# Kernel optimization log

Measured on AMD Instinct MI355X. Metric: run time of the kernel, lower is better.

Reference implementation:

```python
import jax, jax.numpy as jnp
import numpy as np

DIM = 64
H = 4
POS_DIM = 4
NUM_IDS = 16
B = 2048
N = 64


def setup_inputs() -> dict:
    key = jax.random.key(0)
    ks = jax.random.split(key, 16)
    d8 = DIM // 8
    stdv = 1.0 / np.sqrt(DIM * DIM)
    inp = {
        "x": jax.random.normal(ks[0], (B, N, DIM), jnp.float32),
        "pos": jax.random.normal(ks[1], (B, N, POS_DIM), jnp.float32),
        "strength": jax.random.normal(ks[2], (512,), jnp.float32),
        "embed_id1": 3,
        # weights stored [in, out] (torch Linear weight transposed)
        "Wq": jax.random.normal(ks[3], (DIM, DIM), jnp.float32) * 0.05,
        "Wk": jax.random.normal(ks[4], (DIM, DIM), jnp.float32) * 0.05,
        "pos_W1": jax.random.normal(ks[5], (POS_DIM, POS_DIM), jnp.float32) * 0.3,
        "pos_b1": jnp.zeros((POS_DIM,), jnp.float32),
        "pos_W2": jax.random.normal(ks[6], (POS_DIM, d8), jnp.float32) * 0.3,
        "pos_b2": jnp.zeros((d8,), jnp.float32),
        "head_W": jax.random.normal(ks[7], (d8, H), jnp.float32) * 0.3,
        "head_b": jnp.zeros((H,), jnp.float32),
        "gate": jnp.ones((H,), jnp.float32),
        "embeds": jax.random.uniform(ks[8], (NUM_IDS, DIM * DIM), jnp.float32, -stdv, stdv),
        "out_W": jax.random.normal(ks[9], (DIM, DIM), jnp.float32) * 0.05,
        "out_b": jnp.zeros((DIM,), jnp.float32),
        "str_W": jax.random.normal(ks[10], (512, 64), jnp.float32) * 0.04,
        "str_b": jnp.zeros((64,), jnp.float32),
    }
    return inp


def reference(x, pos, strength, embed_id1, Wq, Wk, pos_W1, pos_b1, pos_W2, pos_b2,
              head_W, head_b, gate, embeds, out_W, out_b, str_W, str_b):
    Bb, Nn, dim = x.shape
    h = gate.shape[0]
    dh = dim // h

    # strength projection, added to dynamic-weight V
    s64 = strength @ str_W + str_b                       # [dim]
    E = embeds[embed_id1].reshape(dim, dim)              # per-sample V weight
    v = x @ E.T + s64                                    # F.linear(x, E) + strength
    v = v.reshape(Bb, Nn, h, dh).transpose(0, 2, 1, 3)   # [B,H,N,dh]

    # QK attention
    q = (x @ Wq).reshape(Bb, Nn, h, dh).transpose(0, 2, 1, 3)
    k = (x @ Wk).reshape(Bb, Nn, h, dh).transpose(0, 2, 1, 3)
    attn = jax.nn.softmax(jnp.einsum('bhqd,bhkd->bhqk', q, k) / np.sqrt(dh), axis=-1)

    # pairwise relative-position attention
    p = jax.nn.relu(pos @ pos_W1 + pos_b1) @ pos_W2 + pos_b2          # [B,N,dim//8]
    diff = p[:, :, None, :] - p[:, None, :, :]                        # [B,N,N,dim//8]
    pos_logits = jnp.einsum('bqkf,fh->bhqk', diff, head_W) + head_b[None, :, None, None]
    pos_attn = jax.nn.softmax(pos_logits, axis=-1)

    # sigmoid-gated mixing + renormalization
    g = jax.nn.sigmoid(gate)[None, :, None, None]
    attn = (1.0 - g) * attn + g * pos_attn
    attn = attn / jnp.sum(attn, axis=-1, keepdims=True)

    out = jnp.einsum('bhqk,bhkd->bhqd', attn, v)
    out = out.transpose(0, 2, 1, 3).reshape(Bb, Nn, dim)
    return out @ out_W + out_b
```

## Files before the change

kernel.cpp:

```cpp
#include <hip/hip_runtime.h>

typedef unsigned short u16;
typedef unsigned int u32;
typedef short bf8 __attribute__((ext_vector_type(8)));
typedef float f4v __attribute__((ext_vector_type(4)));
typedef float f16v __attribute__((ext_vector_type(16)));

#define STR 72

__device__ __forceinline__ u32 f2bf(float f){
    union{float f;u32 i;}c; c.f=f; u32 i=c.i;
    return (i + 0x7FFFu + ((i>>16)&1u)) >> 16;
}

__device__ __forceinline__ void stage_row16(const float* __restrict__ g, short* __restrict__ dst,
                                            int n, int c0){
    const float4* p = (const float4*)(g + n*64 + c0);
    float4 a=p[0], b=p[1], c=p[2], d=p[3];
    uint4 o0, o1;
    o0.x = f2bf(a.x)|(f2bf(a.y)<<16); o0.y = f2bf(a.z)|(f2bf(a.w)<<16);
    o0.z = f2bf(b.x)|(f2bf(b.y)<<16); o0.w = f2bf(b.z)|(f2bf(b.w)<<16);
    o1.x = f2bf(c.x)|(f2bf(c.y)<<16); o1.y = f2bf(c.z)|(f2bf(c.w)<<16);
    o1.z = f2bf(d.x)|(f2bf(d.y)<<16); o1.w = f2bf(d.z)|(f2bf(d.w)<<16);
    *(uint4*)&dst[n*STR + c0]     = o0;
    *(uint4*)&dst[n*STR + c0 + 8] = o1;
}

__global__ __launch_bounds__(256) void pre_kernel(
    const int* __restrict__ embed_id,
    const float* __restrict__ Wq, const float* __restrict__ Wk, const float* __restrict__ oW,
    const float* __restrict__ embeds, const float* __restrict__ sW, const float* __restrict__ sb,
    const float* __restrict__ strength,
    float* __restrict__ ws_s64, u16* __restrict__ ws_wq, u16* __restrict__ ws_wk,
    u16* __restrict__ ws_ow, u16* __restrict__ ws_e)
{
    const int j = blockIdx.x;
    const int t = threadIdx.x;

    if (j < 3) {
        const float* W = (j==0) ? Wq : (j==1) ? Wk : oW;
        u16* dst = (j==0) ? ws_wq : (j==1) ? ws_wk : ws_ow;
        const float scl = (j==0) ? 0.25f : 1.0f;
        const int kp = t >> 3, ng = t & 7;
        const float4* r0 = (const float4*)(W + (2*kp  )*64 + 8*ng);
        const float4* r1 = (const float4*)(W + (2*kp+1)*64 + 8*ng);
        float4 a0=r0[0], a1=r0[1], b0=r1[0], b1=r1[1];
        float lo[8]={a0.x,a0.y,a0.z,a0.w,a1.x,a1.y,a1.z,a1.w};
        float hi[8]={b0.x,b0.y,b0.z,b0.w,b1.x,b1.y,b1.z,b1.w};
        #pragma unroll
        for (int i=0;i<8;++i)
            *(u32*)&dst[(8*ng+i)*64 + 2*kp] = f2bf(scl*lo[i]) | (f2bf(scl*hi[i])<<16);
    } else {
        __shared__ float sp[4][64];
        {
            const int n = t >> 2, c0 = (t & 3) << 4;
            const float4* p = (const float4*)(embeds + (size_t)(*embed_id)*4096 + n*64 + c0);
            float4 a=p[0], b=p[1], c=p[2], d=p[3];
            uint4 o0, o1;
            o0.x = f2bf(a.x)|(f2bf(a.y)<<16); o0.y = f2bf(a.z)|(f2bf(a.w)<<16);
            o0.z = f2bf(b.x)|(f2bf(b.y)<<16); o0.w = f2bf(b.z)|(f2bf(b.w)<<16);
            o1.x = f2bf(c.x)|(f2bf(c.y)<<16); o1.y = f2bf(c.z)|(f2bf(c.w)<<16);
            o1.z = f2bf(d.x)|(f2bf(d.y)<<16); o1.w = f2bf(d.z)|(f2bf(d.w)<<16);
            *(uint4*)&ws_e[n*64 + c0]     = o0;
            *(uint4*)&ws_e[n*64 + c0 + 8] = o1;
        }
        {
            const int d = t & 63, part = t >> 6;
            const float* wp = sW + part*128*64 + d;
            const float* s  = strength + part*128;
            float acc = 0.f;
            #pragma unroll 8
            for (int i = 0; i < 128; ++i) acc = fmaf(s[i], wp[i*64], acc);
            sp[part][d] = acc;
        }
        __syncthreads();
        if (t < 64) ws_s64[t] = sp[0][t] + sp[1][t] + sp[2][t] + sp[3][t] + sb[t];
    }
}

__global__ __launch_bounds__(256, 3) void attn_main_kernel(
    const float* __restrict__ x, const float* __restrict__ pos,
    const float* __restrict__ gate, const float* __restrict__ ob,
    const float* __restrict__ pW1, const float* __restrict__ pb1,
    const float* __restrict__ pW2, const float* __restrict__ pb2,
    const float* __restrict__ hW,
    const float* __restrict__ ws_s64,
    const u16* __restrict__ ws_wq, const u16* __restrict__ ws_wk,
    const u16* __restrict__ ws_ow, const u16* __restrict__ ws_e,
    float* __restrict__ out)
{
    __shared__ short B0[64*STR];
    __shared__ short PX[64*STR];
    __shared__ short B2[64*STR];
    __shared__ short B3[64*STR];
    __shared__ short VT[64*STR];
    __shared__ float pat_l[4][64];

    const int t    = threadIdx.x;
    const int b    = blockIdx.x;
    const int lane = t & 63;
    const int w    = t >> 6;
    const int l15  = lane & 15;
    const int l31  = lane & 31;
    const int l5   = lane >> 5;
    const int quad = lane >> 4;
    const int n    = t >> 2;
    const int c0   = (t & 3) << 4;

    const int wq_off = (16*w + l15)*64 + quad*8;
    bf8 bq0 = *(const bf8*)&ws_wq[wq_off];
    bf8 bq1 = *(const bf8*)&ws_wq[wq_off + 32];
    bf8 bk0 = *(const bf8*)&ws_wk[wq_off];
    bf8 bk1 = *(const bf8*)&ws_wk[wq_off + 32];
    bf8 be0 = *(const bf8*)&ws_e [wq_off];
    bf8 be1 = *(const bf8*)&ws_e [wq_off + 32];
    bf8 bo0 = *(const bf8*)&ws_ow[wq_off];
    bf8 bo1 = *(const bf8*)&ws_ow[wq_off + 32];
    const float sv  = ws_s64[16*w + l15];
    const float obv = ob[16*w + l15];

    stage_row16(x + (size_t)b*4096, B0, n, c0);

    float g = 1.f/(1.f + __expf(-gate[w]));
    {
        const float4 pv = *(const float4*)(pos + ((size_t)b*64 + lane)*4);
        float h1[4], p8[8];
        #pragma unroll
        for (int jj = 0; jj < 4; ++jj){
            float a = pb1[jj];
            a = fmaf(pv.x, pW1[0*4+jj], a);
            a = fmaf(pv.y, pW1[1*4+jj], a);
            a = fmaf(pv.z, pW1[2*4+jj], a);
            a = fmaf(pv.w, pW1[3*4+jj], a);
            h1[jj] = fmaxf(a, 0.f);
        }
        #pragma unroll
        for (int f = 0; f < 8; ++f){
            float a = pb2[f];
            #pragma unroll
            for (int jj = 0; jj < 4; ++jj) a = fmaf(h1[jj], pW2[jj*8+f], a);
            p8[f] = a;
        }
        float tv = 0.f;
        #pragma unroll
        for (int f = 0; f < 8; ++f) tv = fmaf(p8[f], hW[f*4+w], tv);
        float v0 = -tv;
        float m = v0;
        #pragma unroll
        for (int off = 32; off; off >>= 1) m = fmaxf(m, __shfl_xor(m, off));
        float e = __expf(v0 - m);
        float ssum = e;
        #pragma unroll
        for (int off = 32; off; off >>= 1) ssum += __shfl_xor(ssum, off);
        pat_l[w][lane] = g * (e / ssum);
    }
    __syncthreads();

    #pragma unroll
    for (int mt=0; mt<4; ++mt){
        bf8 a0 = *(const bf8*)&B0[(16*mt + l15)*STR + quad*8];
        bf8 a1 = *(const bf8*)&B0[(16*mt + l15)*STR + 32 + quad*8];
        f4v cq, ck, cv;
        #pragma unroll
        for (int r=0;r<4;++r){ cq[r]=0.f; ck[r]=0.f; cv[r]=sv; }
        cq = __builtin_amdgcn_mfma_f32_16x16x32_bf16(a0, bq0, cq, 0,0,0);
        cq = __builtin_amdgcn_mfma_f32_16x16x32_bf16(a1, bq1, cq, 0,0,0);
        ck = __builtin_amdgcn_mfma_f32_16x16x32_bf16(a0, bk0, ck, 0,0,0);
        ck = __builtin_amdgcn_mfma_f32_16x16x32_bf16(a1, bk1, ck, 0,0,0);
        cv = __builtin_amdgcn_mfma_f32_16x16x32_bf16(a0, be0, cv, 0,0,0);
        cv = __builtin_amdgcn_mfma_f32_16x16x32_bf16(a1, be1, cv, 0,0,0);
        #pragma unroll
        for (int r=0;r<4;++r){
            B2[(16*mt + quad*4 + r)*STR + 16*w + l15] = (short)f2bf(cq[r]);
            B3[(16*mt + quad*4 + r)*STR + 16*w + l15] = (short)f2bf(ck[r]);
        }
        uint2 pk;
        pk.x = f2bf(cv[0]) | (f2bf(cv[1])<<16);
        pk.y = f2bf(cv[2]) | (f2bf(cv[3])<<16);
        *(uint2*)&VT[(16*w + l15)*STR + 16*mt + quad*4] = pk;
    }
    asm volatile("" ::: "memory");

    f16v S[2][2];
    {
        bf8 ka0 = *(const bf8*)&B3[(     l31)*STR + 16*w + 8*l5];
        bf8 ka1 = *(const bf8*)&B3[(32 + l31)*STR + 16*w + 8*l5];
        bf8 qb0 = *(const bf8*)&B2[(     l31)*STR + 16*w + 8*l5];
        bf8 qb1 = *(const bf8*)&B2[(32 + l31)*STR + 16*w + 8*l5];
        #pragma unroll
        for (int mt=0;mt<2;++mt)
            #pragma unroll
            for (int nt=0;nt<2;++nt)
                #pragma unroll
                for (int i=0;i<16;++i) S[mt][nt][i] = 0.f;
        S[0][0] = __builtin_amdgcn_mfma_f32_32x32x16_bf16(ka0, qb0, S[0][0], 0,0,0);
        S[0][1] = __builtin_amdgcn_mfma_f32_32x32x16_bf16(ka0, qb1, S[0][1], 0,0,0);
        S[1][0] = __builtin_amdgcn_mfma_f32_32x32x16_bf16(ka1, qb0, S[1][0], 0,0,0);
        S[1][1] = __builtin_amdgcn_mfma_f32_32x32x16_bf16(ka1, qb1, S[1][1], 0,0,0);
    }
    float inv_[2];
    #pragma unroll
    for (int nt=0;nt<2;++nt){
        float m = S[0][nt][0];
        #pragma unroll
        for (int i=1;i<16;++i) m = fmaxf(m, S[0][nt][i]);
        #pragma unroll
        for (int i=0;i<16;++i) m = fmaxf(m, S[1][nt][i]);
        m = fmaxf(m, __shfl_xor(m, 32));
        float l = 0.f;
        #pragma unroll
        for (int mt=0;mt<2;++mt)
            #pragma unroll
            for (int i=0;i<16;++i){ float e = __expf(S[mt][nt][i]-m); S[mt][nt][i] = e; l += e; }
        l += __shfl_xor(l, 32);
        float c1 = (1.f - g) / l;
        float tot = 0.f;
        #pragma unroll
        for (int mt=0;mt<2;++mt)
            #pragma unroll
            for (int rg=0;rg<4;++rg){
                const float4 tv = *(const float4*)&pat_l[w][32*mt + 8*rg + 4*l5];
                float a0 = fmaf(c1, S[mt][nt][rg*4+0], tv.x);
                float a1 = fmaf(c1, S[mt][nt][rg*4+1], tv.y);
                float a2 = fmaf(c1, S[mt][nt][rg*4+2], tv.z);
                float a3 = fmaf(c1, S[mt][nt][rg*4+3], tv.w);
                S[mt][nt][rg*4+0]=a0; S[mt][nt][rg*4+1]=a1;
                S[mt][nt][rg*4+2]=a2; S[mt][nt][rg*4+3]=a3;
                tot += a0+a1+a2+a3;
            }
        tot += __shfl_xor(tot, 32);
        inv_[nt] = 1.f / tot;
    }
    __syncthreads();

    short* Pb = (w==0) ? B0 : (w==1) ? PX : (w==2) ? B2 : B3;
    #pragma unroll
    for (int nt=0;nt<2;++nt)
        #pragma unroll
        for (int mt=0;mt<2;++mt)
            #pragma unroll
            for (int rg=0;rg<4;++rg){
                float v0 = S[mt][nt][rg*4+0]*inv_[nt], v1 = S[mt][nt][rg*4+1]*inv_[nt];
                float v2 = S[mt][nt][rg*4+2]*inv_[nt], v3 = S[mt][nt][rg*4+3]*inv_[nt];
                uint2 pk;
                pk.x = f2bf(v0) | (f2bf(v1)<<16);
                pk.y = f2bf(v2) | (f2bf(v3)<<16);
                *(uint2*)&Pb[(32*nt + l31)*STR + 32*mt + 8*rg + 4*l5] = pk;
            }
    asm volatile("" ::: "memory");

    f4v o[4];
    {
        bf8 bv0 = *(const bf8*)&VT[(16*w + l15)*STR + quad*8];
        bf8 bv1 = *(const bf8*)&VT[(16*w + l15)*STR + 32 + quad*8];
        #pragma unroll
        for (int mt=0;mt<4;++mt){
            o[mt][0]=0.f;o[mt][1]=0.f;o[mt][2]=0.f;o[mt][3]=0.f;
            bf8 a0 = *(const bf8*)&Pb[(16*mt + l15)*STR + quad*8];
            bf8 a1 = *(const bf8*)&Pb[(16*mt + l15)*STR + 32 + quad*8];
            o[mt] = __builtin_amdgcn_mfma_f32_16x16x32_bf16(a0, bv0, o[mt], 0,0,0);
            o[mt] = __builtin_amdgcn_mfma_f32_16x16x32_bf16(a1, bv1, o[mt], 0,0,0);
        }
    }
    __syncthreads();

    #pragma unroll
    for (int mt=0;mt<4;++mt)
        #pragma unroll
        for (int r=0;r<4;++r)
            B3[(16*mt + quad*4 + r)*STR + 16*w + l15] = (short)f2bf(o[mt][r]);
    __syncthreads();

    #pragma unroll
    for (int mt=0;mt<4;++mt){
        bf8 ca0 = *(const bf8*)&B3[(16*mt + l15)*STR + quad*8];
        bf8 ca1 = *(const bf8*)&B3[(16*mt + l15)*STR + 32 + quad*8];
        f4v c;
        #pragma unroll
        for (int r=0;r<4;++r) c[r] = obv;
        c = __builtin_amdgcn_mfma_f32_16x16x32_bf16(ca0, bo0, c, 0,0,0);
        c = __builtin_amdgcn_mfma_f32_16x16x32_bf16(ca1, bo1, c, 0,0,0);
        #pragma unroll
        for (int r=0;r<4;++r)
            out[((size_t)b*64 + 16*mt + quad*4 + r)*64 + 16*w + l15] = c[r];
    }
}

extern "C" void kernel_launch(void* const* d_in, const int* in_sizes, int n_in,
                              void* d_out, int out_size, void* d_ws, size_t ws_size,
                              hipStream_t stream) {
    const int B = in_sizes[0] / (64 * 64);

    float* ws_s64 = (float*)d_ws;
    u16*   ws_wq  = (u16*)(ws_s64 + 64);
    u16*   ws_wk  = ws_wq + 4096;
    u16*   ws_ow  = ws_wk + 4096;
    u16*   ws_e   = ws_ow + 4096;

    pre_kernel<<<4, 256, 0, stream>>>(
        (const int*)d_in[3],
        (const float*)d_in[4],  (const float*)d_in[5],  (const float*)d_in[14],
        (const float*)d_in[13], (const float*)d_in[16], (const float*)d_in[17],
        (const float*)d_in[2],
        ws_s64, ws_wq, ws_wk, ws_ow, ws_e);

    attn_main_kernel<<<B, 256, 0, stream>>>(
        (const float*)d_in[0],  (const float*)d_in[1],
        (const float*)d_in[12], (const float*)d_in[15],
        (const float*)d_in[6],  (const float*)d_in[7],  (const float*)d_in[8],  (const float*)d_in[9],
        (const float*)d_in[10],
        ws_s64, ws_wq, ws_wk, ws_ow, ws_e,
        (float*)d_out);
}
```

Before: 138.1 us.

## Persistent blocks loop over batches with register prefetch of next x/pos

The attention kernel becomes persistent: about B/3 blocks each loop over several batch elements, keeping the weight fragments in registers across iterations. Each iteration prefetches the next element's x and pos into registers before the MFMA work and stages them into LDS afterwards, so global-load latency overlaps compute. The position-attention row now lives in spare columns of the VT buffer instead of a separate shared array, which lowers LDS use. The cost is more live registers and fewer resident blocks, which can reduce latency hiding from occupancy.

```diff
diff --git a/kernel.cpp b/kernel.cpp
--- a/kernel.cpp
+++ b/kernel.cpp
@@ -24,6 +24,42 @@
     o1.z = f2bf(d.x)|(f2bf(d.y)<<16); o1.w = f2bf(d.z)|(f2bf(d.w)<<16);
     *(uint4*)&dst[n*STR + c0]     = o0;
     *(uint4*)&dst[n*STR + c0 + 8] = o1;
+}
+
+__device__ __forceinline__ void pat_compute_store(float4 pv, float g, int w, int lane,
+    const float* __restrict__ pW1, const float* __restrict__ pb1,
+    const float* __restrict__ pW2, const float* __restrict__ pb2,
+    const float* __restrict__ hW, short* __restrict__ VT)
+{
+    float h1[4], p8[8];
+    #pragma unroll
+    for (int jj = 0; jj < 4; ++jj){
+        float a = pb1[jj];
+        a = fmaf(pv.x, pW1[0*4+jj], a);
+        a = fmaf(pv.y, pW1[1*4+jj], a);
+        a = fmaf(pv.z, pW1[2*4+jj], a);
+        a = fmaf(pv.w, pW1[3*4+jj], a);
+        h1[jj] = fmaxf(a, 0.f);
+    }
+    #pragma unroll
+    for (int f = 0; f < 8; ++f){
+        float a = pb2[f];
+        #pragma unroll
+        for (int jj = 0; jj < 4; ++jj) a = fmaf(h1[jj], pW2[jj*8+f], a);
+        p8[f] = a;
+    }
+    float tv = 0.f;
+    #pragma unroll
+    for (int f = 0; f < 8; ++f) tv = fmaf(p8[f], hW[f*4+w], tv);
+    float v0 = -tv;
+    float m = v0;
+    #pragma unroll
+    for (int off = 32; off; off >>= 1) m = fmaxf(m, __shfl_xor(m, off));
+    float e = __expf(v0 - m);
+    float ssum = e;
+    #pragma unroll
+    for (int off = 32; off; off >>= 1) ssum += __shfl_xor(ssum, off);
+    *(float*)&VT[(w*16 + (lane>>2))*STR + 64 + (lane&3)*2] = g * (e / ssum);
 }
 
 __global__ __launch_bounds__(256) void pre_kernel(
@@ -87,17 +123,15 @@
     const float* __restrict__ ws_s64,
     const u16* __restrict__ ws_wq, const u16* __restrict__ ws_wk,
     const u16* __restrict__ ws_ow, const u16* __restrict__ ws_e,
-    float* __restrict__ out)
+    float* __restrict__ out, int Btot)
 {
     __shared__ short B0[64*STR];
     __shared__ short PX[64*STR];
     __shared__ short B2[64*STR];
     __shared__ short B3[64*STR];
     __shared__ short VT[64*STR];
-    __shared__ float pat_l[4][64];
 
     const int t    = threadIdx.x;
-    const int b    = blockIdx.x;
     const int lane = t & 63;
     const int w    = t >> 6;
     const int l15  = lane & 15;
@@ -106,6 +140,7 @@
     const int quad = lane >> 4;
     const int n    = t >> 2;
     const int c0   = (t & 3) << 4;
+    const int G    = gridDim.x;
 
     const int wq_off = (16*w + l15)*64 + quad*8;
     bf8 bq0 = *(const bf8*)&ws_wq[wq_off];
@@ -118,171 +153,171 @@
     bf8 bo1 = *(const bf8*)&ws_ow[wq_off + 32];
     const float sv  = ws_s64[16*w + l15];
     const float obv = ob[16*w + l15];
-
-    stage_row16(x + (size_t)b*4096, B0, n, c0);
-
-    float g = 1.f/(1.f + __expf(-gate[w]));
+    const float g   = 1.f/(1.f + __expf(-gate[w]));
+
     {
-        const float4 pv = *(const float4*)(pos + ((size_t)b*64 + lane)*4);
-        float h1[4], p8[8];
-        #pragma unroll
-        for (int jj = 0; jj < 4; ++jj){
-            float a = pb1[jj];
-            a = fmaf(pv.x, pW1[0*4+jj], a);
-            a = fmaf(pv.y, pW1[1*4+jj], a);
-            a = fmaf(pv.z, pW1[2*4+jj], a);
-            a = fmaf(pv.w, pW1[3*4+jj], a);
-            h1[jj] = fmaxf(a, 0.f);
-        }
-        #pragma unroll
-        for (int f = 0; f < 8; ++f){
-            float a = pb2[f];
-            #pragma unroll
-            for (int jj = 0; jj < 4; ++jj) a = fmaf(h1[jj], pW2[jj*8+f], a);
-            p8[f] = a;
-        }
-        float tv = 0.f;
-        #pragma unroll
-        for (int f = 0; f < 8; ++f) tv = fmaf(p8[f], hW[f*4+w], tv);
-        float v0 = -tv;
-        float m = v0;
-        #pragma unroll
-        for (int off = 32; off; off >>= 1) m = fmaxf(m, __shfl_xor(m, off));
-        float e = __expf(v0 - m);
-        float ssum = e;
-        #pragma unroll
-        for (int off = 32; off; off >>= 1) ssum += __shfl_xor(ssum, off);
-        pat_l[w][lane] = g * (e / ssum);
+        const int b0 = blockIdx.x;
+        stage_row16(x + (size_t)b0*4096, B0, n, c0);
+        const float4 pv = *(const float4*)(pos + ((size_t)b0*64 + lane)*4);
+        pat_compute_store(pv, g, w, lane, pW1, pb1, pW2, pb2, hW, VT);
     }
     __syncthreads();
 
-    #pragma unroll
-    for (int mt=0; mt<4; ++mt){
-        bf8 a0 = *(const bf8*)&B0[(16*mt + l15)*STR + quad*8];
-        bf8 a1 = *(const bf8*)&B0[(16*mt + l15)*STR + 32 + quad*8];
-        f4v cq, ck, cv;
-        #pragma unroll
-        for (int r=0;r<4;++r){ cq[r]=0.f; ck[r]=0.f; cv[r]=sv; }
-        cq = __builtin_amdgcn_mfma_f32_16x16x32_bf16(a0, bq0, cq, 0,0,0);
-        cq = __builtin_amdgcn_mfma_f32_16x16x32_bf16(a1, bq1, cq, 0,0,0);
-        ck = __builtin_amdgcn_mfma_f32_16x16x32_bf16(a0, bk0, ck, 0,0,0);
-        ck = __builtin_amdgcn_mfma_f32_16x16x32_bf16(a1, bk1, ck, 0,0,0);
-        cv = __builtin_amdgcn_mfma_f32_16x16x32_bf16(a0, be0, cv, 0,0,0);
-        cv = __builtin_amdgcn_mfma_f32_16x16x32_bf16(a1, be1, cv, 0,0,0);
-        #pragma unroll
-        for (int r=0;r<4;++r){
-            B2[(16*mt + quad*4 + r)*STR + 16*w + l15] = (short)f2bf(cq[r]);
-            B3[(16*mt + quad*4 + r)*STR + 16*w + l15] = (short)f2bf(ck[r]);
-        }
-        uint2 pk;
-        pk.x = f2bf(cv[0]) | (f2bf(cv[1])<<16);
-        pk.y = f2bf(cv[2]) | (f2bf(cv[3])<<16);
-        *(uint2*)&VT[(16*w + l15)*STR + 16*mt + quad*4] = pk;
-    }
-    asm volatile("" ::: "memory");
-
-    f16v S[2][2];
-    {
-        bf8 ka0 = *(const bf8*)&B3[(     l31)*STR + 16*w + 8*l5];
-        bf8 ka1 = *(const bf8*)&B3[(32 + l31)*STR + 16*w + 8*l5];
-        bf8 qb0 = *(const bf8*)&B2[(     l31)*STR + 16*w + 8*l5];
-        bf8 qb1 = *(const bf8*)&B2[(32 + l31)*STR + 16*w + 8*l5];
-        #pragma unroll
-        for (int mt=0;mt<2;++mt)
-            #pragma unroll
-            for (int nt=0;nt<2;++nt)
+    for (int b = blockIdx.x; b < Btot; b += G) {
+        const int  bn   = b + G;
+        const bool hasn = bn < Btot;
+
+        float4 xr0, xr1, xr2, xr3, pr;
+        if (hasn) {
+            const float* gx = x + (size_t)bn*4096 + n*64 + c0;
+            xr0 = *(const float4*)(gx);
+            xr1 = *(const float4*)(gx + 4);
+            xr2 = *(const float4*)(gx + 8);
+            xr3 = *(const float4*)(gx + 12);
+            pr  = *(const float4*)(pos + ((size_t)bn*64 + lane)*4);
+        }
+
+        #pragma unroll
+        for (int mt=0; mt<4; ++mt){
+            bf8 a0 = *(const bf8*)&B0[(16*mt + l15)*STR + quad*8];
+            bf8 a1 = *(const bf8*)&B0[(16*mt + l15)*STR + 32 + quad*8];
+            f4v cq, ck, cv;
+            #pragma unroll
+            for (int r=0;r<4;++r){ cq[r]=0.f; ck[r]=0.f; cv[r]=sv; }
+            cq = __builtin_amdgcn_mfma_f32_16x16x32_bf16(a0, bq0, cq, 0,0,0);
+            cq = __builtin_amdgcn_mfma_f32_16x16x32_bf16(a1, bq1, cq, 0,0,0);
+            ck = __builtin_amdgcn_mfma_f32_16x16x32_bf16(a0, bk0, ck, 0,0,0);
+            ck = __builtin_amdgcn_mfma_f32_16x16x32_bf16(a1, bk1, ck, 0,0,0);
+            cv = __builtin_amdgcn_mfma_f32_16x16x32_bf16(a0, be0, cv, 0,0,0);
+            cv = __builtin_amdgcn_mfma_f32_16x16x32_bf16(a1, be1, cv, 0,0,0);
+            #pragma unroll
+            for (int r=0;r<4;++r){
+                B2[(16*mt + quad*4 + r)*STR + 16*w + l15] = (short)f2bf(cq[r]);
+                B3[(16*mt + quad*4 + r)*STR + 16*w + l15] = (short)f2bf(ck[r]);
+            }
+            uint2 pk;
+            pk.x = f2bf(cv[0]) | (f2bf(cv[1])<<16);
+            pk.y = f2bf(cv[2]) | (f2bf(cv[3])<<16);
+            *(uint2*)&VT[(16*w + l15)*STR + 16*mt + quad*4] = pk;
+        }
+        asm volatile("" ::: "memory");
+
+        f16v S[2][2];
+        {
+            bf8 ka0 = *(const bf8*)&B3[(     l31)*STR + 16*w + 8*l5];
+            bf8 ka1 = *(const bf8*)&B3[(32 + l31)*STR + 16*w + 8*l5];
+            bf8 qb0 = *(const bf8*)&B2[(     l31)*STR + 16*w + 8*l5];
+            bf8 qb1 = *(const bf8*)&B2[(32 + l31)*STR + 16*w + 8*l5];
+            #pragma unroll
+            for (int mt=0;mt<2;++mt)
                 #pragma unroll
-                for (int i=0;i<16;++i) S[mt][nt][i] = 0.f;
-        S[0][0] = __builtin_amdgcn_mfma_f32_32x32x16_bf16(ka0, qb0, S[0][0], 0,0,0);
-        S[0][1] = __builtin_amdgcn_mfma_f32_32x32x16_bf16(ka0, qb1, S[0][1], 0,0,0);
-        S[1][0] = __builtin_amdgcn_mfma_f32_32x32x16_bf16(ka1, qb0, S[1][0], 0,0,0);
-        S[1][1] = __builtin_amdgcn_mfma_f32_32x32x16_bf16(ka1, qb1, S[1][1], 0,0,0);
-    }
-    float inv_[2];
-    #pragma unroll
-    for (int nt=0;nt<2;++nt){
-        float m = S[0][nt][0];
-        #pragma unroll
-        for (int i=1;i<16;++i) m = fmaxf(m, S[0][nt][i]);
-        #pragma unroll
-        for (int i=0;i<16;++i) m = fmaxf(m, S[1][nt][i]);
-        m = fmaxf(m, __shfl_xor(m, 32));
-        float l = 0.f;
-        #pragma unroll
-        for (int mt=0;mt<2;++mt)
-            #pragma unroll
-            for (int i=0;i<16;++i){ float e = __expf(S[mt][nt][i]-m); S[mt][nt][i] = e; l += e; }
-        l += __shfl_xor(l, 32);
-        float c1 = (1.f - g) / l;
-        float tot = 0.f;
-        #pragma unroll
-        for (int mt=0;mt<2;++mt)
-            #pragma unroll
-            for (int rg=0;rg<4;++rg){
-                const float4 tv = *(const float4*)&pat_l[w][32*mt + 8*rg + 4*l5];
-                float a0 = fmaf(c1, S[mt][nt][rg*4+0], tv.x);
-                float a1 = fmaf(c1, S[mt][nt][rg*4+1], tv.y);
-                float a2 = fmaf(c1, S[mt][nt][rg*4+2], tv.z);
-                float a3 = fmaf(c1, S[mt][nt][rg*4+3], tv.w);
-                S[mt][nt][rg*4+0]=a0; S[mt][nt][rg*4+1]=a1;
-                S[mt][nt][rg*4+2]=a2; S[mt][nt][rg*4+3]=a3;
-                tot += a0+a1+a2+a3;
+                for (int nt=0;nt<2;++nt)
+                    #pragma unroll
+                    for (int i=0;i<16;++i) S[mt][nt][i] = 0.f;
+            S[0][0] = __builtin_amdgcn_mfma_f32_32x32x16_bf16(ka0, qb0, S[0][0], 0,0,0);
+            S[0][1] = __builtin_amdgcn_mfma_f32_32x32x16_bf16(ka0, qb1, S[0][1], 0,0,0);
+            S[1][0] = __builtin_amdgcn_mfma_f32_32x32x16_bf16(ka1, qb0, S[1][0], 0,0,0);
+            S[1][1] = __builtin_amdgcn_mfma_f32_32x32x16_bf16(ka1, qb1, S[1][1], 0,0,0);
+        }
+        float inv_[2];
+        #pragma unroll
+        for (int nt=0;nt<2;++nt){
+            float m = S[0][nt][0];
+            #pragma unroll
+            for (int i=1;i<16;++i) m = fmaxf(m, S[0][nt][i]);
+            #pragma unroll
+            for (int i=0;i<16;++i) m = fmaxf(m, S[1][nt][i]);
+            m = fmaxf(m, __shfl_xor(m, 32));
+            float l = 0.f;
+            #pragma unroll
+            for (int mt=0;mt<2;++mt)
+                #pragma unroll
+                for (int i=0;i<16;++i){ float e = __expf(S[mt][nt][i]-m); S[mt][nt][i] = e; l += e; }
+            l += __shfl_xor(l, 32);
+            float c1 = (1.f - g) / l;
+            float tot = 0.f;
+            #pragma unroll
+            for (int mt=0;mt<2;++mt)
+                #pragma unroll
+                for (int rg=0;rg<4;++rg){
+                    const float4 tv = *(const float4*)&VT[(w*16 + 8*mt + 2*rg + l5)*STR + 64];
+                    float a0 = fmaf(c1, S[mt][nt][rg*4+0], tv.x);
+                    float a1 = fmaf(c1, S[mt][nt][rg*4+1], tv.y);
+                    float a2 = fmaf(c1, S[mt][nt][rg*4+2], tv.z);
+                    float a3 = fmaf(c1, S[mt][nt][rg*4+3], tv.w);
+                    S[mt][nt][rg*4+0]=a0; S[mt][nt][rg*4+1]=a1;
+                    S[mt][nt][rg*4+2]=a2; S[mt][nt][rg*4+3]=a3;
+                    tot += a0+a1+a2+a3;
+                }
+            tot += __shfl_xor(tot, 32);
+            inv_[nt] = 1.f / tot;
+        }
+        __syncthreads();
+
+        short* Pb = (w==0) ? B0 : (w==1) ? PX : (w==2) ? B2 : B3;
+        #pragma unroll
+        for (int nt=0;nt<2;++nt)
+            #pragma unroll
+            for (int mt=0;mt<2;++mt)
+                #pragma unroll
+                for (int rg=0;rg<4;++rg){
+                    float v0 = S[mt][nt][rg*4+0]*inv_[nt], v1 = S[mt][nt][rg*4+1]*inv_[nt];
+                    float v2 = S[mt][nt][rg*4+2]*inv_[nt], v3 = S[mt][nt][rg*4+3]*inv_[nt];
+                    uint2 pk;
+                    pk.x = f2bf(v0) | (f2bf(v1)<<16);
+                    pk.y = f2bf(v2) | (f2bf(v3)<<16);
+                    *(uint2*)&Pb[(32*nt + l31)*STR + 32*mt + 8*rg + 4*l5] = pk;
+                }
+        asm volatile("" ::: "memory");
+
+        f4v o[4];
+        {
+            bf8 bv0 = *(const bf8*)&VT[(16*w + l15)*STR + quad*8];
+            bf8 bv1 = *(const bf8*)&VT[(16*w + l15)*STR + 32 + quad*8];
+            #pragma unroll
+            for (int mt=0;mt<4;++mt){
+                o[mt][0]=0.f;o[mt][1]=0.f;o[mt][2]=0.f;o[mt][3]=0.f;
+                bf8 a0 = *(const bf8*)&Pb[(16*mt + l15)*STR + quad*8];
+                bf8 a1 = *(const bf8*)&Pb[(16*mt + l15)*STR + 32 + quad*8];
+                o[mt] = __builtin_amdgcn_mfma_f32_16x16x32_bf16(a0, bv0, o[mt], 0,0,0);
+                o[mt] = __builtin_amdgcn_mfma_f32_16x16x32_bf16(a1, bv1, o[mt], 0,0,0);
             }
-        tot += __shfl_xor(tot, 32);
-        inv_[nt] = 1.f / tot;
-    }
-    __syncthreads();
-
-    short* Pb = (w==0) ? B0 : (w==1) ? PX : (w==2) ? B2 : B3;
-    #pragma unroll
-    for (int nt=0;nt<2;++nt)
-        #pragma unroll
-        for (int mt=0;mt<2;++mt)
-            #pragma unroll
-            for (int rg=0;rg<4;++rg){
-                float v0 = S[mt][nt][rg*4+0]*inv_[nt], v1 = S[mt][nt][rg*4+1]*inv_[nt];
-                float v2 = S[mt][nt][rg*4+2]*inv_[nt], v3 = S[mt][nt][rg*4+3]*inv_[nt];
-                uint2 pk;
-                pk.x = f2bf(v0) | (f2bf(v1)<<16);
-                pk.y = f2bf(v2) | (f2bf(v3)<<16);
-                *(uint2*)&Pb[(32*nt + l31)*STR + 32*mt + 8*rg + 4*l5] = pk;
-            }
-    asm volatile("" ::: "memory");
-
-    f4v o[4];
-    {
-        bf8 bv0 = *(const bf8*)&VT[(16*w + l15)*STR + quad*8];
-        bf8 bv1 = *(const bf8*)&VT[(16*w + l15)*STR + 32 + quad*8];
+        }
+        __syncthreads();
+
+        if (hasn) {
+            uint4 o0, o1;
+            o0.x = f2bf(xr0.x)|(f2bf(xr0.y)<<16); o0.y = f2bf(xr0.z)|(f2bf(xr0.w)<<16);
+            o0.z = f2bf(xr1.x)|(f2bf(xr1.y)<<16); o0.w = f2bf(xr1.z)|(f2bf(xr1.w)<<16);
+            o1.x = f2bf(xr2.x)|(f2bf(xr2.y)<<16); o1.y = f2bf(xr2.z)|(f2bf(xr2.w)<<16);
+            o1.z = f2bf(xr3.x)|(f2bf(xr3.y)<<16); o1.w = f2bf(xr3.z)|(f2bf(xr3.w)<<16);
+            *(uint4*)&B0[n*STR + c0]     = o0;
+            *(uint4*)&B0[n*STR + c0 + 8] = o1;
+            pat_compute_store(pr, g, w, lane, pW1, pb1, pW2, pb2, hW, VT);
+        }
+
+        #pragma unroll
+        for (int mt=0;mt<4;++mt)
+            #pragma unroll
+            for (int r=0;r<4;++r)
+                B3[(16*mt + quad*4 + r)*STR + 16*w + l15] = (short)f2bf(o[mt][r]);
+        __syncthreads();
+
         #pragma unroll
         for (int mt=0;mt<4;++mt){
-            o[mt][0]=0.f;o[mt][1]=0.f;o[mt][2]=0.f;o[mt][3]=0.f;
-            bf8 a0 = *(const bf8*)&Pb[(16*mt + l15)*STR + quad*8];
-            bf8 a1 = *(const bf8*)&Pb[(16*mt + l15)*STR + 32 + quad*8];
-            o[mt] = __builtin_amdgcn_mfma_f32_16x16x32_bf16(a0, bv0, o[mt], 0,0,0);
-            o[mt] = __builtin_amdgcn_mfma_f32_16x16x32_bf16(a1, bv1, o[mt], 0,0,0);
-        }
-    }
-    __syncthreads();
-
-    #pragma unroll
-    for (int mt=0;mt<4;++mt)
-        #pragma unroll
-        for (int r=0;r<4;++r)
-            B3[(16*mt + quad*4 + r)*STR + 16*w + l15] = (short)f2bf(o[mt][r]);
-    __syncthreads();
-
-    #pragma unroll
-    for (int mt=0;mt<4;++mt){
-        bf8 ca0 = *(const bf8*)&B3[(16*mt + l15)*STR + quad*8];
-        bf8 ca1 = *(const bf8*)&B3[(16*mt + l15)*STR + 32 + quad*8];
-        f4v c;
-        #pragma unroll
-        for (int r=0;r<4;++r) c[r] = obv;
-        c = __builtin_amdgcn_mfma_f32_16x16x32_bf16(ca0, bo0, c, 0,0,0);
-        c = __builtin_amdgcn_mfma_f32_16x16x32_bf16(ca1, bo1, c, 0,0,0);
-        #pragma unroll
-        for (int r=0;r<4;++r)
-            out[((size_t)b*64 + 16*mt + quad*4 + r)*64 + 16*w + l15] = c[r];
+            bf8 ca0 = *(const bf8*)&B3[(16*mt + l15)*STR + quad*8];
+            bf8 ca1 = *(const bf8*)&B3[(16*mt + l15)*STR + 32 + quad*8];
+            f4v c;
+            #pragma unroll
+            for (int r=0;r<4;++r) c[r] = obv;
+            c = __builtin_amdgcn_mfma_f32_16x16x32_bf16(ca0, bo0, c, 0,0,0);
+            c = __builtin_amdgcn_mfma_f32_16x16x32_bf16(ca1, bo1, c, 0,0,0);
+            #pragma unroll
+            for (int r=0;r<4;++r)
+                out[((size_t)b*64 + 16*mt + quad*4 + r)*64 + 16*w + l15] = c[r];
+        }
+
+        if (hasn) __syncthreads();
     }
 }
 
@@ -304,11 +339,12 @@
         (const float*)d_in[2],
         ws_s64, ws_wq, ws_wk, ws_ow, ws_e);
 
-    attn_main_kernel<<<B, 256, 0, stream>>>(
+    const int grid = (B + 2) / 3;
+    attn_main_kernel<<<grid, 256, 0, stream>>>(
         (const float*)d_in[0],  (const float*)d_in[1],
         (const float*)d_in[12], (const float*)d_in[15],
         (const float*)d_in[6],  (const float*)d_in[7],  (const float*)d_in[8],  (const float*)d_in[9],
         (const float*)d_in[10],
         ws_s64, ws_wq, ws_wk, ws_ow, ws_e,
-        (float*)d_out);
-}
+        (float*)d_out, B);
+}
```

After: 187.3 us. 1.36x slower.

## Fold position attention into a rank-one term, swizzle LDS, use hardware bf16 packing

Applied to the files above, without the earlier changes.

The renormalisation is dropped because each mixed row already sums to one. The key-only position softmax is turned into a per-column vector pg = sum_k pat[k]*v[k], added to the PV output, so only the QK softmax probabilities go through the PV MFMA. LDS padding (stride 72) is replaced by an XOR swizzle, which shrinks shared memory so the occupancy hint can rise from 3 to 4 blocks per CU. Software bf16 rounding is replaced by the v_cvt_pk_bf16_f32 instruction. The risks are small numeric differences from summing the position term in fp32 outside the bf16 matmul, and swizzle indexing mistakes.

```diff
diff --git a/kernel.cpp b/kernel.cpp
--- a/kernel.cpp
+++ b/kernel.cpp
@@ -6,11 +6,20 @@
 typedef float f4v __attribute__((ext_vector_type(4)));
 typedef float f16v __attribute__((ext_vector_type(16)));
 
-#define STR 72
-
 __device__ __forceinline__ u32 f2bf(float f){
     union{float f;u32 i;}c; c.f=f; u32 i=c.i;
     return (i + 0x7FFFu + ((i>>16)&1u)) >> 16;
+}
+
+__device__ __forceinline__ u32 cvtpk(float lo, float hi){
+    u32 r; asm("v_cvt_pk_bf16_f32 %0, %1, %2" : "=v"(r) : "v"(lo), "v"(hi)); return r;
+}
+__device__ __forceinline__ short cvt1(float v){
+    u32 r; asm("v_cvt_pk_bf16_f32 %0, %1, %2" : "=v"(r) : "v"(v), "v"(v)); return (short)r;
+}
+
+__device__ __forceinline__ int sx(int row, int colbyte){
+    return row*64 + ((colbyte ^ ((row & 7) << 4)) >> 1);
 }
 
 __device__ __forceinline__ void stage_row16(const float* __restrict__ g, short* __restrict__ dst,
@@ -18,12 +27,12 @@
     const float4* p = (const float4*)(g + n*64 + c0);
     float4 a=p[0], b=p[1], c=p[2], d=p[3];
     uint4 o0, o1;
-    o0.x = f2bf(a.x)|(f2bf(a.y)<<16); o0.y = f2bf(a.z)|(f2bf(a.w)<<16);
-    o0.z = f2bf(b.x)|(f2bf(b.y)<<16); o0.w = f2bf(b.z)|(f2bf(b.w)<<16);
-    o1.x = f2bf(c.x)|(f2bf(c.y)<<16); o1.y = f2bf(c.z)|(f2bf(c.w)<<16);
-    o1.z = f2bf(d.x)|(f2bf(d.y)<<16); o1.w = f2bf(d.z)|(f2bf(d.w)<<16);
-    *(uint4*)&dst[n*STR + c0]     = o0;
-    *(uint4*)&dst[n*STR + c0 + 8] = o1;
+    o0.x = cvtpk(a.x,a.y); o0.y = cvtpk(a.z,a.w);
+    o0.z = cvtpk(b.x,b.y); o0.w = cvtpk(b.z,b.w);
+    o1.x = cvtpk(c.x,c.y); o1.y = cvtpk(c.z,c.w);
+    o1.z = cvtpk(d.x,d.y); o1.w = cvtpk(d.z,d.w);
+    *(uint4*)&dst[sx(n, 2*c0)]      = o0;
+    *(uint4*)&dst[sx(n, 2*c0 + 16)] = o1;
 }
 
 __global__ __launch_bounds__(256) void pre_kernel(
@@ -78,7 +87,7 @@
     }
 }
 
-__global__ __launch_bounds__(256, 3) void attn_main_kernel(
+__global__ __launch_bounds__(256, 4) void attn_main_kernel(
     const float* __restrict__ x, const float* __restrict__ pos,
     const float* __restrict__ gate, const float* __restrict__ ob,
     const float* __restrict__ pW1, const float* __restrict__ pb1,
@@ -89,12 +98,11 @@
     const u16* __restrict__ ws_ow, const u16* __restrict__ ws_e,
     float* __restrict__ out)
 {
-    __shared__ short B0[64*STR];
-    __shared__ short PX[64*STR];
-    __shared__ short B2[64*STR];
-    __shared__ short B3[64*STR];
-    __shared__ short VT[64*STR];
-    __shared__ float pat_l[4][64];
+    __shared__ short B0[64*64];
+    __shared__ short PX[64*64];
+    __shared__ short B2[64*64];
+    __shared__ short B3[64*64];
+    __shared__ short VT[64*64];
 
     const int t    = threadIdx.x;
     const int b    = blockIdx.x;
@@ -118,10 +126,11 @@
     bf8 bo1 = *(const bf8*)&ws_ow[wq_off + 32];
     const float sv  = ws_s64[16*w + l15];
     const float obv = ob[16*w + l15];
+    const float g   = 1.f/(1.f + __expf(-gate[w]));
 
     stage_row16(x + (size_t)b*4096, B0, n, c0);
 
-    float g = 1.f/(1.f + __expf(-gate[w]));
+    float patk;
     {
         const float4 pv = *(const float4*)(pos + ((size_t)b*64 + lane)*4);
         float h1[4], p8[8];
@@ -152,14 +161,15 @@
         float ssum = e;
         #pragma unroll
         for (int off = 32; off; off >>= 1) ssum += __shfl_xor(ssum, off);
-        pat_l[w][lane] = g * (e / ssum);
+        patk = g * (e / ssum);
     }
     __syncthreads();
 
+    float pg = 0.f;
     #pragma unroll
     for (int mt=0; mt<4; ++mt){
-        bf8 a0 = *(const bf8*)&B0[(16*mt + l15)*STR + quad*8];
-        bf8 a1 = *(const bf8*)&B0[(16*mt + l15)*STR + 32 + quad*8];
+        bf8 a0 = *(const bf8*)&B0[sx(16*mt + l15, 16*quad)];
+        bf8 a1 = *(const bf8*)&B0[sx(16*mt + l15, 64 + 16*quad)];
         f4v cq, ck, cv;
         #pragma unroll
         for (int r=0;r<4;++r){ cq[r]=0.f; ck[r]=0.f; cv[r]=sv; }
@@ -171,22 +181,25 @@
         cv = __builtin_amdgcn_mfma_f32_16x16x32_bf16(a1, be1, cv, 0,0,0);
         #pragma unroll
         for (int r=0;r<4;++r){
-            B2[(16*mt + quad*4 + r)*STR + 16*w + l15] = (short)f2bf(cq[r]);
-            B3[(16*mt + quad*4 + r)*STR + 16*w + l15] = (short)f2bf(ck[r]);
+            B2[sx(16*mt + 4*quad + r, 2*(16*w + l15))] = cvt1(cq[r]);
+            B3[sx(16*mt + 4*quad + r, 2*(16*w + l15))] = cvt1(ck[r]);
+            pg = fmaf(__shfl(patk, 16*mt + 4*quad + r), cv[r], pg);
         }
         uint2 pk;
-        pk.x = f2bf(cv[0]) | (f2bf(cv[1])<<16);
-        pk.y = f2bf(cv[2]) | (f2bf(cv[3])<<16);
-        *(uint2*)&VT[(16*w + l15)*STR + 16*mt + quad*4] = pk;
-    }
+        pk.x = cvtpk(cv[0], cv[1]);
+        pk.y = cvtpk(cv[2], cv[3]);
+        *(uint2*)&VT[sx(16*w + l15, 32*mt + 8*quad)] = pk;
+    }
+    pg += __shfl_xor(pg, 16);
+    pg += __shfl_xor(pg, 32);
     asm volatile("" ::: "memory");
 
     f16v S[2][2];
     {
-        bf8 ka0 = *(const bf8*)&B3[(     l31)*STR + 16*w + 8*l5];
-        bf8 ka1 = *(const bf8*)&B3[(32 + l31)*STR + 16*w + 8*l5];
-        bf8 qb0 = *(const bf8*)&B2[(     l31)*STR + 16*w + 8*l5];
-        bf8 qb1 = *(const bf8*)&B2[(32 + l31)*STR + 16*w + 8*l5];
+        bf8 ka0 = *(const bf8*)&B3[sx(     l31, 32*w + 16*l5)];
+        bf8 ka1 = *(const bf8*)&B3[sx(32 + l31, 32*w + 16*l5)];
+        bf8 qb0 = *(const bf8*)&B2[sx(     l31, 32*w + 16*l5)];
+        bf8 qb1 = *(const bf8*)&B2[sx(32 + l31, 32*w + 16*l5)];
         #pragma unroll
         for (int mt=0;mt<2;++mt)
             #pragma unroll
@@ -198,7 +211,7 @@
         S[1][0] = __builtin_amdgcn_mfma_f32_32x32x16_bf16(ka1, qb0, S[1][0], 0,0,0);
         S[1][1] = __builtin_amdgcn_mfma_f32_32x32x16_bf16(ka1, qb1, S[1][1], 0,0,0);
     }
-    float inv_[2];
+    float c1_[2];
     #pragma unroll
     for (int nt=0;nt<2;++nt){
         float m = S[0][nt][0];
@@ -213,51 +226,35 @@
             #pragma unroll
             for (int i=0;i<16;++i){ float e = __expf(S[mt][nt][i]-m); S[mt][nt][i] = e; l += e; }
         l += __shfl_xor(l, 32);
-        float c1 = (1.f - g) / l;
-        float tot = 0.f;
+        c1_[nt] = (1.f - g) / l;
+    }
+    __syncthreads();
+
+    short* Pb = (w==0) ? B0 : (w==1) ? PX : (w==2) ? B2 : B3;
+    #pragma unroll
+    for (int nt=0;nt<2;++nt)
         #pragma unroll
         for (int mt=0;mt<2;++mt)
             #pragma unroll
             for (int rg=0;rg<4;++rg){
-                const float4 tv = *(const float4*)&pat_l[w][32*mt + 8*rg + 4*l5];
-                float a0 = fmaf(c1, S[mt][nt][rg*4+0], tv.x);
-                float a1 = fmaf(c1, S[mt][nt][rg*4+1], tv.y);
-                float a2 = fmaf(c1, S[mt][nt][rg*4+2], tv.z);
-                float a3 = fmaf(c1, S[mt][nt][rg*4+3], tv.w);
-                S[mt][nt][rg*4+0]=a0; S[mt][nt][rg*4+1]=a1;
-                S[mt][nt][rg*4+2]=a2; S[mt][nt][rg*4+3]=a3;
-                tot += a0+a1+a2+a3;
-            }
-        tot += __shfl_xor(tot, 32);
-        inv_[nt] = 1.f / tot;
-    }
-    __syncthreads();
-
-    short* Pb = (w==0) ? B0 : (w==1) ? PX : (w==2) ? B2 : B3;
-    #pragma unroll
-    for (int nt=0;nt<2;++nt)
-        #pragma unroll
-        for (int mt=0;mt<2;++mt)
-            #pragma unroll
-            for (int rg=0;rg<4;++rg){
-                float v0 = S[mt][nt][rg*4+0]*inv_[nt], v1 = S[mt][nt][rg*4+1]*inv_[nt];
-                float v2 = S[mt][nt][rg*4+2]*inv_[nt], v3 = S[mt][nt][rg*4+3]*inv_[nt];
+                float v0 = S[mt][nt][rg*4+0]*c1_[nt], v1 = S[mt][nt][rg*4+1]*c1_[nt];
+                float v2 = S[mt][nt][rg*4+2]*c1_[nt], v3 = S[mt][nt][rg*4+3]*c1_[nt];
                 uint2 pk;
-                pk.x = f2bf(v0) | (f2bf(v1)<<16);
-                pk.y = f2bf(v2) | (f2bf(v3)<<16);
-                *(uint2*)&Pb[(32*nt + l31)*STR + 32*mt + 8*rg + 4*l5] = pk;
+                pk.x = cvtpk(v0, v1);
+                pk.y = cvtpk(v2, v3);
+                *(uint2*)&Pb[sx(32*nt + l31, 64*mt + 16*rg + 8*l5)] = pk;
             }
     asm volatile("" ::: "memory");
 
     f4v o[4];
     {
-        bf8 bv0 = *(const bf8*)&VT[(16*w + l15)*STR + quad*8];
-        bf8 bv1 = *(const bf8*)&VT[(16*w + l15)*STR + 32 + quad*8];
+        bf8 bv0 = *(const bf8*)&VT[sx(16*w + l15, 16*quad)];
+        bf8 bv1 = *(const bf8*)&VT[sx(16*w + l15, 64 + 16*quad)];
         #pragma unroll
         for (int mt=0;mt<4;++mt){
             o[mt][0]=0.f;o[mt][1]=0.f;o[mt][2]=0.f;o[mt][3]=0.f;
-            bf8 a0 = *(const bf8*)&Pb[(16*mt + l15)*STR + quad*8];
-            bf8 a1 = *(const bf8*)&Pb[(16*mt + l15)*STR + 32 + quad*8];
+            bf8 a0 = *(const bf8*)&Pb[sx(16*mt + l15, 16*quad)];
+            bf8 a1 = *(const bf8*)&Pb[sx(16*mt + l15, 64 + 16*quad)];
             o[mt] = __builtin_amdgcn_mfma_f32_16x16x32_bf16(a0, bv0, o[mt], 0,0,0);
             o[mt] = __builtin_amdgcn_mfma_f32_16x16x32_bf16(a1, bv1, o[mt], 0,0,0);
         }
@@ -268,13 +265,13 @@
     for (int mt=0;mt<4;++mt)
         #pragma unroll
         for (int r=0;r<4;++r)
-            B3[(16*mt + quad*4 + r)*STR + 16*w + l15] = (short)f2bf(o[mt][r]);
+            B3[sx(16*mt + 4*quad + r, 2*(16*w + l15))] = cvt1(o[mt][r] + pg);
     __syncthreads();
 
     #pragma unroll
     for (int mt=0;mt<4;++mt){
-        bf8 ca0 = *(const bf8*)&B3[(16*mt + l15)*STR + quad*8];
-        bf8 ca1 = *(const bf8*)&B3[(16*mt + l15)*STR + 32 + quad*8];
+        bf8 ca0 = *(const bf8*)&B3[sx(16*mt + l15, 16*quad)];
+        bf8 ca1 = *(const bf8*)&B3[sx(16*mt + l15, 64 + 16*quad)];
         f4v c;
         #pragma unroll
         for (int r=0;r<4;++r) c[r] = obv;
```

Result: no change. 139.9 us (+1.3%).
